# Kernel optimization log

Measured on AMD Instinct MI355X. Metric: run time of the kernel, lower is better.

## Reference

```python
import jax, jax.numpy as jnp
import numpy as np

N = 100000   # nodes
E = 1600000  # directed edges
HID = 64


def gat_conv(x, src, dst, W, a_src, a_dst, b, heads, out_ch):
    """PyG-style GATConv (add_self_loops=True, negative_slope=0.2, concat)."""
    n = x.shape[0]
    h = (x @ W).reshape(n, heads, out_ch)              # [N,H,C]
    loop = jnp.arange(n, dtype=src.dtype)
    s = jnp.concatenate([src, loop])                   # self loops appended
    d = jnp.concatenate([dst, loop])
    alpha_src = jnp.sum(h * a_src, axis=-1)            # [N,H]
    alpha_dst = jnp.sum(h * a_dst, axis=-1)            # [N,H]
    alpha = jax.nn.leaky_relu(alpha_src[s] + alpha_dst[d], 0.2)  # [E+N,H]
    # segment softmax over incoming edges of each destination node
    amax = jax.ops.segment_max(alpha, d, num_segments=n)
    alpha = jnp.exp(alpha - amax[d])
    asum = jax.ops.segment_sum(alpha, d, num_segments=n)
    alpha = alpha / (asum[d] + 1e-16)
    msg = h[s] * alpha[:, :, None]                     # [E+N,H,C]
    out = jax.ops.segment_sum(msg, d, num_segments=n)  # [N,H,C]
    return out.reshape(n, heads * out_ch) + b


def setup_inputs() -> dict:
    key = jax.random.key(0)
    ks = jax.random.split(key, 22)
    rn = lambda k, shp, s=0.1: (jax.random.normal(k, shp, jnp.float32) * s)
    inp = {
        "x": jax.random.normal(ks[0], (N, 2), jnp.float32),
        "edge_index": jax.random.randint(ks[1], (2, E), 0, N, dtype=jnp.int32),
        "edge_attr": jax.random.normal(ks[2], (E, 2), jnp.float32),
        # node encoder
        "enc_W": rn(ks[3], (2, HID)), "enc_b": rn(ks[4], (HID,)),
        # gat1: heads=4, out=16
        "g1_W": rn(ks[5], (HID, HID)), "g1_as": rn(ks[6], (4, 16)),
        "g1_ad": rn(ks[7], (4, 16)), "g1_b": rn(ks[8], (HID,)),
        # gat2: heads=1, out=64
        "g2_W": rn(ks[9], (HID, HID)), "g2_as": rn(ks[10], (1, HID)),
        "g2_ad": rn(ks[11], (1, HID)), "g2_b": rn(ks[12], (HID,)),
        # node head
        "no_W1": rn(ks[13], (HID, HID)), "no_b1": rn(ks[14], (HID,)),
        "no_W2": rn(ks[15], (HID, 2)), "no_b2": rn(ks[16], (2,)),
        # edge head: in = 2*HID + 2 = 130
        "eo_W1": rn(ks[17], (2 * HID + 2, HID)), "eo_b1": rn(ks[18], (HID,)),
        "eo_W2": rn(ks[19], (HID, 1)), "eo_b2": rn(ks[20], (1,)),
    }
    return inp


def reference(x, edge_index, edge_attr, enc_W, enc_b,
              g1_W, g1_as, g1_ad, g1_b,
              g2_W, g2_as, g2_ad, g2_b,
              no_W1, no_b1, no_W2, no_b2,
              eo_W1, eo_b1, eo_W2, eo_b2):
    src, dst = edge_index[0], edge_index[1]
    h = x @ enc_W + enc_b                                    # node encoder (dropout = eval identity)
    h = jax.nn.elu(gat_conv(h, src, dst, g1_W, g1_as, g1_ad, g1_b, 4, 16))
    h = gat_conv(h, src, dst, g2_W, g2_as, g2_ad, g2_b, 1, HID)
    e_in = jnp.concatenate([h[src], h[dst], edge_attr], axis=-1)  # [E,130]
    node_pred = jnp.tanh(jax.nn.leaky_relu(h @ no_W1 + no_b1, 0.01) @ no_W2 + no_b2)
    edge_pred = jnp.tanh(jax.nn.leaky_relu(e_in @ eo_W1 + eo_b1, 0.01) @ eo_W2 + eo_b2)[:, 0]
    return edge_pred, node_pred
```

## Files before the change

kernel.cpp:

```cpp
#include <hip/hip_runtime.h>
#include <hip/hip_fp16.h>
#include <math.h>


typedef _Float16 half8_t __attribute__((ext_vector_type(8)));
typedef float floatx4 __attribute__((ext_vector_type(4)));

__global__ void k_init_cursors(int* cursor, int NB, int cap){
  int b = blockIdx.x * blockDim.x + threadIdx.x;
  if (b < NB) cursor[b] = b * cap;
}

__global__ void k_scatter(const int* __restrict__ src, const int* __restrict__ dst,
                          int E, int NB, int cap, int* cursor,
                          unsigned int* __restrict__ ebuf){
  __shared__ int hist[256];
  __shared__ int base[256];
  int t = threadIdx.x;
  hist[t] = 0;
  __syncthreads();
  int cbase = blockIdx.x * 2048;
  int sv[8], bk[8], dl[8];
  #pragma unroll
  for (int i = 0; i < 8; ++i){
    int e = cbase + i * 256 + t;
    if (e < E){
      int d = dst[e];
      sv[i] = src[e]; bk[i] = d >> 9; dl[i] = d & 511;
      atomicAdd(&hist[bk[i]], 1);
    } else bk[i] = -1;
  }
  __syncthreads();
  int c = hist[t];
  base[t] = (t < NB && c > 0) ? atomicAdd(&cursor[t], c) : 0;
  __syncthreads();
  hist[t] = 0;
  __syncthreads();
  #pragma unroll
  for (int i = 0; i < 8; ++i){
    if (bk[i] >= 0){
      int r = atomicAdd(&hist[bk[i]], 1);
      int p = base[bk[i]] + r;
      if (p < (bk[i] + 1) * cap)
        ebuf[p] = (unsigned)sv[i] | ((unsigned)dl[i] << 17);
    }
  }
}

__global__ void k_bucket_build(const int* __restrict__ cursor, int cap, int N,
                               unsigned int* ebuf, int* __restrict__ rstart,
                               int* __restrict__ rend){
  __shared__ unsigned int ent[12288];
  __shared__ int cnts[512];
  __shared__ int aux[512];
  int b = blockIdx.x, t = threadIdx.x;
  int base = b * cap;
  int cnt = cursor[b] - base;
  if (cnt > cap) cnt = cap;
  for (int i = t; i < cnt; i += 512) ent[i] = ebuf[base + i];
  cnts[t] = 0;
  __syncthreads();
  for (int i = t; i < cnt; i += 512) atomicAdd(&cnts[ent[i] >> 17], 1);
  __syncthreads();
  int v = cnts[t];
  aux[t] = v;
  __syncthreads();
  for (int off = 1; off < 512; off <<= 1){
    int x = (t >= off) ? aux[t - off] : 0;
    __syncthreads();
    aux[t] += x;
    __syncthreads();
  }
  int incl = aux[t];
  int node = (b << 9) + t;
  if (node < N){ rstart[node] = base + incl - v; rend[node] = base + incl; }
  cnts[t] = incl - v;
  __syncthreads();
  for (int i = t; i < cnt; i += 512){
    unsigned int en = ent[i];
    int pos = atomicAdd(&cnts[en >> 17], 1);
    ebuf[base + pos] = en & 0x1FFFFu;
  }
}

__global__ void k_precompute(const float* __restrict__ encW, const float* __restrict__ encb,
                             const float* __restrict__ g1W, float* __restrict__ Mc){
  int j = threadIdx.x;
  if (j >= 64) return;
  float m0 = 0.f, m1 = 0.f, cc = 0.f;
  for (int t = 0; t < 64; ++t){
    float g = g1W[t * 64 + j];
    m0 = fmaf(encW[t], g, m0);
    m1 = fmaf(encW[64 + t], g, m1);
    cc = fmaf(encb[t], g, cc);
  }
  Mc[j] = m0; Mc[64 + j] = m1; Mc[128 + j] = cc;
}

__global__ void k_fuse1(const float* __restrict__ x, const float* __restrict__ Mc,
                        const float* __restrict__ a_s, const float* __restrict__ a_d,
                        __half* __restrict__ hw, float* __restrict__ alpha_s,
                        float* __restrict__ alpha_d, int n){
  int idx = blockIdx.x * blockDim.x + threadIdx.x;
  if (idx >= n * 64) return;
  int node = idx >> 6, j = idx & 63;
  float acc = fmaf(x[node * 2 + 0], Mc[j], fmaf(x[node * 2 + 1], Mc[64 + j], Mc[128 + j]));
  hw[idx] = __float2half(acc);
  float ps = acc * a_s[j];
  float pd = acc * a_d[j];
  #pragma unroll
  for (int off = 1; off < 16; off <<= 1){
    ps += __shfl_xor(ps, off);
    pd += __shfl_xor(pd, off);
  }
  if ((j & 15) == 0){
    int h = j >> 4;
    alpha_s[node * 4 + h] = ps;
    alpha_d[node * 4 + h] = pd;
  }
}

__global__ __launch_bounds__(256) void k_hw_mfma(
    const float* __restrict__ hin, const float* __restrict__ W,
    const float* __restrict__ a_s, const float* __restrict__ a_d,
    __half* __restrict__ hw, float* __restrict__ alpha_s,
    float* __restrict__ alpha_d, int n){
  __shared__ float redS[4][16];
  __shared__ float redD[4][16];
  int t = threadIdx.x;
  int lane = t & 63, wave = t >> 6;
  int l15 = lane & 15, quad = lane >> 4;
  int ch = wave * 16 + l15;
  half8_t b0, b1;
  #pragma unroll
  for (int j = 0; j < 8; ++j){
    b0[j] = (_Float16)W[(quad * 8 + j) * 64 + ch];
    b1[j] = (_Float16)W[(quad * 8 + j + 32) * 64 + ch];
  }
  float asv = a_s[ch], adv = a_d[ch];
  int base = blockIdx.x * 64;
  for (int it = 0; it < 4; ++it){
    int tb = base + it * 16;
    if (tb >= n) break;
    int arn = tb + l15; if (arn >= n) arn = n - 1;
    const float* arow = hin + (size_t)arn * 64 + quad * 8;
    half8_t a0, a1;
    #pragma unroll
    for (int j = 0; j < 8; ++j){
      a0[j] = (_Float16)arow[j];
      a1[j] = (_Float16)arow[j + 32];
    }
    floatx4 acc = {0.f, 0.f, 0.f, 0.f};
    acc = __builtin_amdgcn_mfma_f32_16x16x32_f16(a0, b0, acc, 0, 0, 0);
    acc = __builtin_amdgcn_mfma_f32_16x16x32_f16(a1, b1, acc, 0, 0, 0);
    float ps[4], pd[4];
    #pragma unroll
    for (int r = 0; r < 4; ++r){
      int node = tb + quad * 4 + r;
      if (node < n) hw[(size_t)node * 64 + ch] = __float2half(acc[r]);
      ps[r] = acc[r] * asv;
      pd[r] = acc[r] * adv;
      #pragma unroll
      for (int off = 1; off < 16; off <<= 1){
        ps[r] += __shfl_xor(ps[r], off);
        pd[r] += __shfl_xor(pd[r], off);
      }
    }
    if (l15 == 0){
      #pragma unroll
      for (int r = 0; r < 4; ++r){
        redS[wave][quad * 4 + r] = ps[r];
        redD[wave][quad * 4 + r] = pd[r];
      }
    }
    __syncthreads();
    if (t < 16 && tb + t < n){
      alpha_s[tb + t] = redS[0][t] + redS[1][t] + redS[2][t] + redS[3][t];
      alpha_d[tb + t] = redD[0][t] + redD[1][t] + redD[2][t] + redD[3][t];
    }
    __syncthreads();
  }
}

template<int H, bool ELU_ACT>
__global__ void k_agg(const __half* __restrict__ hw, const float* __restrict__ alpha_s,
                      const float* __restrict__ alpha_d, const int* __restrict__ rstart,
                      const int* __restrict__ rend, const int* __restrict__ col,
                      const float* __restrict__ bias, float* __restrict__ hout, int n){
  int node = (blockIdx.x * blockDim.x + threadIdx.x) >> 6;
  int lane = threadIdx.x & 63;
  int g = lane >> 4, c = lane & 15;
  if (node >= n) return;
  int hidx = (c * H) >> 4;
  float adn = alpha_d[node * H + hidx];
  int start = rstart[node], end = rend[node];
  float acc0 = 0.f, acc1 = 0.f, acc2 = 0.f, acc3 = 0.f, psum = 0.f;
  if (g == 0){
    float a = alpha_s[node * H + hidx] + adn;
    a = a > 0.f ? a : 0.2f * a;
    float p = __expf(a);
    psum = p;
    float2 rv = *(const float2*)(hw + (size_t)node * 64 + c * 4);
    const __half2* hp = (const __half2*)&rv;
    float2 f0 = __half22float2(hp[0]), f1 = __half22float2(hp[1]);
    acc0 = p * f0.x; acc1 = p * f0.y; acc2 = p * f1.x; acc3 = p * f1.y;
  }
  for (int i = start + g; i < end; i += 4){
    int s = col[i];
    float a = alpha_s[s * H + hidx] + adn;
    a = a > 0.f ? a : 0.2f * a;
    float p = __expf(a);
    float2 rv = *(const float2*)(hw + (size_t)s * 64 + c * 4);
    const __half2* hp = (const __half2*)&rv;
    float2 f0 = __half22float2(hp[0]), f1 = __half22float2(hp[1]);
    psum += p;
    acc0 = fmaf(p, f0.x, acc0);
    acc1 = fmaf(p, f0.y, acc1);
    acc2 = fmaf(p, f1.x, acc2);
    acc3 = fmaf(p, f1.y, acc3);
  }
  #pragma unroll
  for (int off = 16; off < 64; off <<= 1){
    psum += __shfl_xor(psum, off);
    acc0 += __shfl_xor(acc0, off);
    acc1 += __shfl_xor(acc1, off);
    acc2 += __shfl_xor(acc2, off);
    acc3 += __shfl_xor(acc3, off);
  }
  if (g == 0){
    float inv = 1.f / (psum + 1e-16f);
    float4 bv = ((const float4*)bias)[c];
    float o0 = fmaf(acc0, inv, bv.x);
    float o1 = fmaf(acc1, inv, bv.y);
    float o2 = fmaf(acc2, inv, bv.z);
    float o3 = fmaf(acc3, inv, bv.w);
    if (ELU_ACT){
      o0 = o0 > 0.f ? o0 : (__expf(o0) - 1.f);
      o1 = o1 > 0.f ? o1 : (__expf(o1) - 1.f);
      o2 = o2 > 0.f ? o2 : (__expf(o2) - 1.f);
      o3 = o3 > 0.f ? o3 : (__expf(o3) - 1.f);
    }
    float4 ov = {o0, o1, o2, o3};
    *(float4*)(hout + (size_t)node * 64 + c * 4) = ov;
  }
}

__global__ __launch_bounds__(256) void k_heads_mfma(
    const float* __restrict__ h, const float* __restrict__ eoW1,
    const float* __restrict__ noW1, const float* __restrict__ nob1,
    const float* __restrict__ noW2, const float* __restrict__ nob2,
    __half* __restrict__ P1, __half* __restrict__ P2,
    float* __restrict__ outN, int n){
  __shared__ float redP[4][16][2];
  int t = threadIdx.x;
  int lane = t & 63, wave = t >> 6;
  int l15 = lane & 15, quad = lane >> 4;
  int ch = wave * 16 + l15;
  half8_t bP1a, bP1b, bP2a, bP2b, bNa, bNb;
  #pragma unroll
  for (int j = 0; j < 8; ++j){
    int k0 = quad * 8 + j, k1 = k0 + 32;
    bP1a[j] = (_Float16)eoW1[k0 * 64 + ch];
    bP1b[j] = (_Float16)eoW1[k1 * 64 + ch];
    bP2a[j] = (_Float16)eoW1[(k0 + 64) * 64 + ch];
    bP2b[j] = (_Float16)eoW1[(k1 + 64) * 64 + ch];
    bNa[j]  = (_Float16)noW1[k0 * 64 + ch];
    bNb[j]  = (_Float16)noW1[k1 * 64 + ch];
  }
  float b1v = nob1[ch];
  float w20 = noW2[ch * 2 + 0], w21 = noW2[ch * 2 + 1];
  float b20 = nob2[0], b21 = nob2[1];
  int base = blockIdx.x * 64;
  for (int it = 0; it < 4; ++it){
    int tb = base + it * 16;
    if (tb >= n) break;
    int arn = tb + l15; if (arn >= n) arn = n - 1;
    const float* arow = h + (size_t)arn * 64 + quad * 8;
    half8_t a0, a1;
    #pragma unroll
    for (int j = 0; j < 8; ++j){
      a0[j] = (_Float16)arow[j];
      a1[j] = (_Float16)arow[j + 32];
    }
    floatx4 ac1 = {0.f,0.f,0.f,0.f}, ac2 = {0.f,0.f,0.f,0.f}, acN = {0.f,0.f,0.f,0.f};
    ac1 = __builtin_amdgcn_mfma_f32_16x16x32_f16(a0, bP1a, ac1, 0, 0, 0);
    ac1 = __builtin_amdgcn_mfma_f32_16x16x32_f16(a1, bP1b, ac1, 0, 0, 0);
    ac2 = __builtin_amdgcn_mfma_f32_16x16x32_f16(a0, bP2a, ac2, 0, 0, 0);
    ac2 = __builtin_amdgcn_mfma_f32_16x16x32_f16(a1, bP2b, ac2, 0, 0, 0);
    acN = __builtin_amdgcn_mfma_f32_16x16x32_f16(a0, bNa, acN, 0, 0, 0);
    acN = __builtin_amdgcn_mfma_f32_16x16x32_f16(a1, bNb, acN, 0, 0, 0);
    float p0[4], p1[4];
    #pragma unroll
    for (int r = 0; r < 4; ++r){
      int node = tb + quad * 4 + r;
      if (node < n){
        P1[(size_t)node * 64 + ch] = __float2half(ac1[r]);
        P2[(size_t)node * 64 + ch] = __float2half(ac2[r]);
      }
      float v = acN[r] + b1v;
      v = v > 0.f ? v : 0.01f * v;
      p0[r] = v * w20;
      p1[r] = v * w21;
      #pragma unroll
      for (int off = 1; off < 16; off <<= 1){
        p0[r] += __shfl_xor(p0[r], off);
        p1[r] += __shfl_xor(p1[r], off);
      }
    }
    if (l15 == 0){
      #pragma unroll
      for (int r = 0; r < 4; ++r){
        redP[wave][quad * 4 + r][0] = p0[r];
        redP[wave][quad * 4 + r][1] = p1[r];
      }
    }
    __syncthreads();
    if (t < 16 && tb + t < n){
      float s0 = redP[0][t][0] + redP[1][t][0] + redP[2][t][0] + redP[3][t][0];
      float s1 = redP[0][t][1] + redP[1][t][1] + redP[2][t][1] + redP[3][t][1];
      outN[(size_t)(tb + t) * 2 + 0] = tanhf(s0 + b20);
      outN[(size_t)(tb + t) * 2 + 1] = tanhf(s1 + b21);
    }
    __syncthreads();
  }
}

__global__ void k_edge_head(const __half* __restrict__ P1h, const __half* __restrict__ P2h,
                            const int* __restrict__ src, const int* __restrict__ dst,
                            const float* __restrict__ eattr, const float* __restrict__ eoW1,
                            const float* __restrict__ b1, const float* __restrict__ W2,
                            const float* __restrict__ b2, float* __restrict__ out, int E){
  int lane = threadIdx.x & 63;
  int jj = lane & 7, q = lane >> 3;
  int wid = (blockIdx.x * blockDim.x + threadIdx.x) >> 6;
  int nw = (gridDim.x * blockDim.x) >> 6;

  const float4* rAq = (const float4*)(eoW1 + 8192);
  const float4* rBq = (const float4*)(eoW1 + 8256);
  const float4* b1q = (const float4*)b1;
  const float4* w2q = (const float4*)W2;
  float4 tA0 = rAq[2 * jj], tA1 = rAq[2 * jj + 1];
  float4 tB0 = rBq[2 * jj], tB1 = rBq[2 * jj + 1];
  float4 tb0 = b1q[2 * jj], tb1 = b1q[2 * jj + 1];
  float4 tw0 = w2q[2 * jj], tw1 = w2q[2 * jj + 1];
  float ra[8] = {tA0.x, tA0.y, tA0.z, tA0.w, tA1.x, tA1.y, tA1.z, tA1.w};
  float rb[8] = {tB0.x, tB0.y, tB0.z, tB0.w, tB1.x, tB1.y, tB1.z, tB1.w};
  float bb[8] = {tb0.x, tb0.y, tb0.z, tb0.w, tb1.x, tb1.y, tb1.z, tb1.w};
  float w2[8] = {tw0.x, tw0.y, tw0.z, tw0.w, tw1.x, tw1.y, tw1.z, tw1.w};
  float b2v = b2[0];

  const float4* P1q = (const float4*)P1h;
  const float4* P2q = (const float4*)P2h;
  const float2* eav = (const float2*)eattr;

  int groups = (E + 7) >> 3;
  for (int g = wid; g < groups; g += nw){
    int e = g * 8 + q;
    bool act = (e < E);
    float p = 0.f;
    if (act){
      int s = src[e], d = dst[e];
      float2 ea = eav[e];
      float4 g1 = P1q[(size_t)s * 8 + jj];
      float4 g2 = P2q[(size_t)d * 8 + jj];
      const __half2* h1 = (const __half2*)&g1;
      const __half2* h2 = (const __half2*)&g2;
      float v[8];
      #pragma unroll
      for (int k = 0; k < 4; ++k){
        float2 u = __half22float2(h1[k]);
        float2 w = __half22float2(h2[k]);
        v[2 * k]     = u.x + w.x;
        v[2 * k + 1] = u.y + w.y;
      }
      #pragma unroll
      for (int k = 0; k < 8; ++k){
        float t = v[k] + bb[k];
        t = fmaf(ea.x, ra[k], fmaf(ea.y, rb[k], t));
        t = t > 0.f ? t : 0.01f * t;
        p = fmaf(t, w2[k], p);
      }
    }
    #pragma unroll
    for (int off = 1; off < 8; off <<= 1) p += __shfl_xor(p, off);
    if (jj == 0 && act) out[e] = tanhf(p + b2v);
  }
}

extern "C" void kernel_launch(void* const* d_in, const int* in_sizes, int n_in,
                              void* d_out, int out_size, void* d_ws, size_t ws_size,
                              hipStream_t stream){
  const float* x    = (const float*)d_in[0];
  const int*   eidx = (const int*)  d_in[1];
  const float* ea   = (const float*)d_in[2];
  const float* encW = (const float*)d_in[3];
  const float* encb = (const float*)d_in[4];
  const float* g1W  = (const float*)d_in[5];
  const float* g1as = (const float*)d_in[6];
  const float* g1ad = (const float*)d_in[7];
  const float* g1b  = (const float*)d_in[8];
  const float* g2W  = (const float*)d_in[9];
  const float* g2as = (const float*)d_in[10];
  const float* g2ad = (const float*)d_in[11];
  const float* g2b  = (const float*)d_in[12];
  const float* noW1 = (const float*)d_in[13];
  const float* nob1 = (const float*)d_in[14];
  const float* noW2 = (const float*)d_in[15];
  const float* nob2 = (const float*)d_in[16];
  const float* eoW1 = (const float*)d_in[17];
  const float* eob1 = (const float*)d_in[18];
  const float* eoW2 = (const float*)d_in[19];
  const float* eob2 = (const float*)d_in[20];

  const int N = in_sizes[0] / 2;
  const int E = in_sizes[1] / 2;
  const int* src = eidx;
  const int* dst = eidx + E;

  const int NB = (N + 511) >> 9;
  int avg = (E + NB - 1) / NB;
  int cap = avg + avg / 4 + 64;
  if (cap > 12288) cap = 12288;

  char* ws = (char*)d_ws;
  size_t off = 0;
  auto alloc = [&](size_t bytes) -> void* {
    void* p = ws + off;
    off = (off + bytes + 255) & ~(size_t)255;
    return p;
  };
  float*  bufA  = (float*) alloc((size_t)N * 64 * 4);
  __half* bufH  = (__half*)alloc((size_t)N * 64 * 2);
  __half* P1h   = (__half*)alloc((size_t)N * 64 * 2);
  __half* P2h   = (__half*)alloc((size_t)N * 64 * 2);
  float*  as    = (float*) alloc((size_t)N * 4 * 4);
  float*  ad    = (float*) alloc((size_t)N * 4 * 4);
  int* rstart   = (int*)   alloc((size_t)N * 4);
  int* rend     = (int*)   alloc((size_t)N * 4);
  unsigned int* ebuf = (unsigned int*)alloc((size_t)NB * cap * 4);
  int* cursor   = (int*)   alloc((size_t)NB * 4);
  float* Mc     = (float*) alloc(192 * 4);

  k_init_cursors<<<(NB + 255) / 256, 256, 0, stream>>>(cursor, NB, cap);
  k_scatter<<<(E + 2047) / 2048, 256, 0, stream>>>(src, dst, E, NB, cap, cursor, ebuf);
  k_bucket_build<<<NB, 512, 0, stream>>>(cursor, cap, N, ebuf, rstart, rend);
  const int* col = (const int*)ebuf;

  k_precompute<<<1, 64, 0, stream>>>(encW, encb, g1W, Mc);
  k_fuse1<<<(N * 64 + 255) / 256, 256, 0, stream>>>(x, Mc, g1as, g1ad, bufH, as, ad, N);
  k_agg<4, true><<<(N + 3) / 4, 256, 0, stream>>>(bufH, as, ad, rstart, rend, col, g1b, bufA, N);

  k_hw_mfma<<<(N + 63) / 64, 256, 0, stream>>>(bufA, g2W, g2as, g2ad, bufH, as, ad, N);
  k_agg<1, false><<<(N + 3) / 4, 256, 0, stream>>>(bufH, as, ad, rstart, rend, col, g2b, bufA, N);

  float* out = (float*)d_out;
  k_heads_mfma<<<(N + 63) / 64, 256, 0, stream>>>(bufA, eoW1, noW1, nob1, noW2, nob2,
                                                  P1h, P2h, out + E, N);
  k_edge_head<<<2048, 256, 0, stream>>>(P1h, P2h, src, dst, ea,
                                        eoW1, eob1, eoW2, eob2, out, E);
}
```

Before: 398.4 us.

## Precompute per-edge attention exponentials in CSR build and unroll aggregation loop

Moves edge attention computation (leaky-relu plus exp of alpha_s[src]+alpha_d[dst]) out of the aggregation kernels. For layer 1 it is fused into the bucket build, which now runs after the node projection. For layer 2 a separate pass computes it. The aggregation loop reads these precomputed values contiguously and is unrolled by two. Separately, the precompute kernel is folded into the scatter kernel and cursor init becomes a memset. The aim is to remove random alpha_s gathers and exp work from the latency-bound gather loop, at the cost of writing and reading a per-edge float4 buffer (E*16 bytes) and one extra kernel pass.

```diff
diff --git a/kernel.cpp b/kernel.cpp
--- a/kernel.cpp
+++ b/kernel.cpp
@@ -6,17 +6,24 @@
 typedef _Float16 half8_t __attribute__((ext_vector_type(8)));
 typedef float floatx4 __attribute__((ext_vector_type(4)));
 
-__global__ void k_init_cursors(int* cursor, int NB, int cap){
-  int b = blockIdx.x * blockDim.x + threadIdx.x;
-  if (b < NB) cursor[b] = b * cap;
-}
-
 __global__ void k_scatter(const int* __restrict__ src, const int* __restrict__ dst,
                           int E, int NB, int cap, int* cursor,
-                          unsigned int* __restrict__ ebuf){
+                          unsigned int* __restrict__ ebuf,
+                          const float* __restrict__ encW, const float* __restrict__ encb,
+                          const float* __restrict__ g1W, float* __restrict__ Mc){
   __shared__ int hist[256];
   __shared__ int base[256];
   int t = threadIdx.x;
+  if (blockIdx.x == 0 && t < 64){
+    float m0 = 0.f, m1 = 0.f, cc = 0.f;
+    for (int k = 0; k < 64; ++k){
+      float g = g1W[k * 64 + t];
+      m0 = fmaf(encW[k], g, m0);
+      m1 = fmaf(encW[64 + k], g, m1);
+      cc = fmaf(encb[k], g, cc);
+    }
+    Mc[t] = m0; Mc[64 + t] = m1; Mc[128 + t] = cc;
+  }
   hist[t] = 0;
   __syncthreads();
   int cbase = blockIdx.x * 2048;
@@ -32,7 +39,7 @@
   }
   __syncthreads();
   int c = hist[t];
-  base[t] = (t < NB && c > 0) ? atomicAdd(&cursor[t], c) : 0;
+  base[t] = (t < NB && c > 0) ? (t * cap + atomicAdd(&cursor[t], c)) : 0;
   __syncthreads();
   hist[t] = 0;
   __syncthreads();
@@ -49,13 +56,16 @@
 
 __global__ void k_bucket_build(const int* __restrict__ cursor, int cap, int N,
                                unsigned int* ebuf, int* __restrict__ rstart,
-                               int* __restrict__ rend){
+                               int* __restrict__ rend,
+                               const float* __restrict__ as4,
+                               const float* __restrict__ ad4,
+                               float4* __restrict__ palpha4){
   __shared__ unsigned int ent[12288];
   __shared__ int cnts[512];
   __shared__ int aux[512];
   int b = blockIdx.x, t = threadIdx.x;
   int base = b * cap;
-  int cnt = cursor[b] - base;
+  int cnt = cursor[b];
   if (cnt > cap) cnt = cap;
   for (int i = t; i < cnt; i += 512) ent[i] = ebuf[base + i];
   cnts[t] = 0;
@@ -78,23 +88,40 @@
   __syncthreads();
   for (int i = t; i < cnt; i += 512){
     unsigned int en = ent[i];
-    int pos = atomicAdd(&cnts[en >> 17], 1);
-    ebuf[base + pos] = en & 0x1FFFFu;
-  }
-}
-
-__global__ void k_precompute(const float* __restrict__ encW, const float* __restrict__ encb,
-                             const float* __restrict__ g1W, float* __restrict__ Mc){
-  int j = threadIdx.x;
-  if (j >= 64) return;
-  float m0 = 0.f, m1 = 0.f, cc = 0.f;
-  for (int t = 0; t < 64; ++t){
-    float g = g1W[t * 64 + j];
-    m0 = fmaf(encW[t], g, m0);
-    m1 = fmaf(encW[64 + t], g, m1);
-    cc = fmaf(encb[t], g, cc);
-  }
-  Mc[j] = m0; Mc[64 + j] = m1; Mc[128 + j] = cc;
+    int dl = en >> 17;
+    int s = en & 0x1FFFFu;
+    int pos = atomicAdd(&cnts[dl], 1);
+    ebuf[base + pos] = en;
+    int d = (b << 9) + dl;
+    float4 sv = ((const float4*)as4)[s];
+    float4 dv = ((const float4*)ad4)[d];
+    float a0 = sv.x + dv.x, a1 = sv.y + dv.y, a2 = sv.z + dv.z, a3 = sv.w + dv.w;
+    a0 = a0 > 0.f ? a0 : 0.2f * a0;
+    a1 = a1 > 0.f ? a1 : 0.2f * a1;
+    a2 = a2 > 0.f ? a2 : 0.2f * a2;
+    a3 = a3 > 0.f ? a3 : 0.2f * a3;
+    float4 pv = {__expf(a0), __expf(a1), __expf(a2), __expf(a3)};
+    palpha4[base + pos] = pv;
+  }
+}
+
+__global__ void k_palpha1(const int* __restrict__ cursor, int cap,
+                          const unsigned int* __restrict__ ebuf,
+                          const float* __restrict__ as, const float* __restrict__ ad,
+                          float* __restrict__ palpha1){
+  int blk = blockIdx.x;
+  int b = blk >> 2, part = blk & 3;
+  int base = b * cap;
+  int cnt = cursor[b];
+  if (cnt > cap) cnt = cap;
+  for (int i = part * 256 + threadIdx.x; i < cnt; i += 1024){
+    unsigned int en = ebuf[base + i];
+    int s = en & 0x1FFFFu;
+    int d = (b << 9) + (en >> 17);
+    float a = as[s] + ad[d];
+    a = a > 0.f ? a : 0.2f * a;
+    palpha1[base + i] = __expf(a);
+  }
 }
 
 __global__ void k_fuse1(const float* __restrict__ x, const float* __restrict__ Mc,
@@ -183,20 +210,20 @@
 }
 
 template<int H, bool ELU_ACT>
-__global__ void k_agg(const __half* __restrict__ hw, const float* __restrict__ alpha_s,
-                      const float* __restrict__ alpha_d, const int* __restrict__ rstart,
-                      const int* __restrict__ rend, const int* __restrict__ col,
+__global__ void k_agg(const __half* __restrict__ hw, const float* __restrict__ palpha,
+                      const float* __restrict__ alpha_s, const float* __restrict__ alpha_d,
+                      const int* __restrict__ rstart, const int* __restrict__ rend,
+                      const unsigned int* __restrict__ ebuf,
                       const float* __restrict__ bias, float* __restrict__ hout, int n){
   int node = (blockIdx.x * blockDim.x + threadIdx.x) >> 6;
   int lane = threadIdx.x & 63;
   int g = lane >> 4, c = lane & 15;
   if (node >= n) return;
   int hidx = (c * H) >> 4;
-  float adn = alpha_d[node * H + hidx];
   int start = rstart[node], end = rend[node];
   float acc0 = 0.f, acc1 = 0.f, acc2 = 0.f, acc3 = 0.f, psum = 0.f;
   if (g == 0){
-    float a = alpha_s[node * H + hidx] + adn;
+    float a = alpha_s[node * H + hidx] + alpha_d[node * H + hidx];
     a = a > 0.f ? a : 0.2f * a;
     float p = __expf(a);
     psum = p;
@@ -205,11 +232,27 @@
     float2 f0 = __half22float2(hp[0]), f1 = __half22float2(hp[1]);
     acc0 = p * f0.x; acc1 = p * f0.y; acc2 = p * f1.x; acc3 = p * f1.y;
   }
-  for (int i = start + g; i < end; i += 4){
-    int s = col[i];
-    float a = alpha_s[s * H + hidx] + adn;
-    a = a > 0.f ? a : 0.2f * a;
-    float p = __expf(a);
+  int i = start + g;
+  for (; i + 4 < end; i += 8){
+    int s0 = ebuf[i] & 0x1FFFF;
+    int s1 = ebuf[i + 4] & 0x1FFFF;
+    float p0 = palpha[(size_t)i * H + hidx];
+    float p1 = palpha[(size_t)(i + 4) * H + hidx];
+    float2 rv0 = *(const float2*)(hw + (size_t)s0 * 64 + c * 4);
+    float2 rv1 = *(const float2*)(hw + (size_t)s1 * 64 + c * 4);
+    const __half2* h0 = (const __half2*)&rv0;
+    const __half2* h1 = (const __half2*)&rv1;
+    float2 a0 = __half22float2(h0[0]), b0 = __half22float2(h0[1]);
+    float2 a1 = __half22float2(h1[0]), b1 = __half22float2(h1[1]);
+    psum += p0 + p1;
+    acc0 = fmaf(p0, a0.x, fmaf(p1, a1.x, acc0));
+    acc1 = fmaf(p0, a0.y, fmaf(p1, a1.y, acc1));
+    acc2 = fmaf(p0, b0.x, fmaf(p1, b1.x, acc2));
+    acc3 = fmaf(p0, b0.y, fmaf(p1, b1.y, acc3));
+  }
+  if (i < end){
+    int s = ebuf[i] & 0x1FFFF;
+    float p = palpha[(size_t)i * H + hidx];
     float2 rv = *(const float2*)(hw + (size_t)s * 64 + c * 4);
     const __half2* hp = (const __half2*)&rv;
     float2 f0 = __half22float2(hp[0]), f1 = __half22float2(hp[1]);
@@ -438,21 +481,22 @@
   int* rstart   = (int*)   alloc((size_t)N * 4);
   int* rend     = (int*)   alloc((size_t)N * 4);
   unsigned int* ebuf = (unsigned int*)alloc((size_t)NB * cap * 4);
+  float4* palpha4 = (float4*)alloc((size_t)NB * cap * 16);
+  float* palpha1  = (float*)palpha4;
   int* cursor   = (int*)   alloc((size_t)NB * 4);
   float* Mc     = (float*) alloc(192 * 4);
 
-  k_init_cursors<<<(NB + 255) / 256, 256, 0, stream>>>(cursor, NB, cap);
-  k_scatter<<<(E + 2047) / 2048, 256, 0, stream>>>(src, dst, E, NB, cap, cursor, ebuf);
-  k_bucket_build<<<NB, 512, 0, stream>>>(cursor, cap, N, ebuf, rstart, rend);
-  const int* col = (const int*)ebuf;
-
-  k_precompute<<<1, 64, 0, stream>>>(encW, encb, g1W, Mc);
+  hipMemsetAsync(cursor, 0, (size_t)NB * 4, stream);
+  k_scatter<<<(E + 2047) / 2048, 256, 0, stream>>>(src, dst, E, NB, cap, cursor, ebuf,
+                                                   encW, encb, g1W, Mc);
   k_fuse1<<<(N * 64 + 255) / 256, 256, 0, stream>>>(x, Mc, g1as, g1ad, bufH, as, ad, N);
-  k_agg<4, true><<<(N + 3) / 4, 256, 0, stream>>>(bufH, as, ad, rstart, rend, col, g1b, bufA, N);
-
+  k_bucket_build<<<NB, 512, 0, stream>>>(cursor, cap, N, ebuf, rstart, rend, as, ad, palpha4);
+  k_agg<4, true><<<(N + 3) / 4, 256, 0, stream>>>(bufH, (const float*)palpha4, as, ad,
+                                                  rstart, rend, ebuf, g1b, bufA, N);
   k_hw_mfma<<<(N + 63) / 64, 256, 0, stream>>>(bufA, g2W, g2as, g2ad, bufH, as, ad, N);
-  k_agg<1, false><<<(N + 3) / 4, 256, 0, stream>>>(bufH, as, ad, rstart, rend, col, g2b, bufA, N);
-
+  k_palpha1<<<NB * 4, 256, 0, stream>>>(cursor, cap, ebuf, as, ad, palpha1);
+  k_agg<1, false><<<(N + 3) / 4, 256, 0, stream>>>(bufH, palpha1, as, ad,
+                                                   rstart, rend, ebuf, g2b, bufA, N);
   float* out = (float*)d_out;
   k_heads_mfma<<<(N + 63) / 64, 256, 0, stream>>>(bufA, eoW1, noW1, nob1, noW2, nob2,
                                                   P1h, P2h, out + E, N);
```

After: 402.1 us. Within noise of the previous version (+0.9%).
